# Kernel tuning notes

Hardware: AMD Instinct MI355X
Metric: run time of the kernel (lower is better)

## Reference

```python
import jax, jax.numpy as jnp
import numpy as np

B, N, DIM, MV = 8, 16384, 512, 8
SCALE = 0.1
EPS = 1e-5


def _cayley():
    # Cl(3,0) basis order: 1, e1, e2, e3, e12, e13, e23, e123 (bitmasks below)
    masks = [0b000, 0b001, 0b010, 0b100, 0b011, 0b101, 0b110, 0b111]
    idx = {m: i for i, m in enumerate(masks)}
    C = np.zeros((8, 8, 8), dtype=np.float32)
    for i, a in enumerate(masks):
        for j, b in enumerate(masks):
            s, aa = 0, a >> 1
            while aa:  # reordering sign; Euclidean signature so squares are +1
                s += bin(aa & b).count('1')
                aa >>= 1
            C[i, j, idx[a ^ b]] = -1.0 if (s % 2) else 1.0
    return jnp.asarray(C)


def setup_inputs() -> dict:
    key = jax.random.key(0)
    ks = jax.random.split(key, 8)
    lim_in = 1.0 / np.sqrt(DIM)
    lim_out = 1.0 / np.sqrt(MV)
    x = jax.random.normal(ks[0], (B, N, DIM), dtype=jnp.float32)
    Wp = jax.random.uniform(ks[1], (MV, DIM), minval=-lim_in, maxval=lim_in, dtype=jnp.float32)
    bp = jax.random.uniform(ks[2], (MV,), minval=-lim_in, maxval=lim_in, dtype=jnp.float32)
    Wm = jax.random.uniform(ks[3], (MV, DIM), minval=-lim_in, maxval=lim_in, dtype=jnp.float32)
    bm = jax.random.uniform(ks[4], (MV,), minval=-lim_in, maxval=lim_in, dtype=jnp.float32)
    Wo = jax.random.uniform(ks[5], (DIM, MV), minval=-lim_out, maxval=lim_out, dtype=jnp.float32)
    bo = jax.random.uniform(ks[6], (DIM,), minval=-lim_out, maxval=lim_out, dtype=jnp.float32)
    gamma = jnp.ones((DIM,), dtype=jnp.float32)
    beta = jnp.zeros((DIM,), dtype=jnp.float32)
    return {"x": x, "Wp": Wp, "bp": bp, "Wm": Wm, "bm": bm,
            "Wo": Wo, "bo": bo, "gamma": gamma, "beta": beta}


def reference(x, Wp, bp, Wm, bm, Wo, bo, gamma, beta):
    C = _cayley()  # [8,8,8] sparse Cayley tensor for Cl(3,0)
    particle_mv = jnp.einsum('bnd,md->bnm', x, Wp) + bp          # [B,N,8]
    mean_field = x.mean(axis=1)                                   # [B,D]
    meanfield_mv = jnp.einsum('bd,md->bm', mean_field, Wm) + bm   # [B,8]
    # geometric product: mean-field mv is shared across N
    product = jnp.einsum('bni,ijk,bj->bnk', particle_mv, C, meanfield_mv)  # [B,N,8]
    out = jnp.einsum('bnk,dk->bnd', product, Wo) + bo             # [B,N,D]
    y = x + SCALE * out
    mu = y.mean(axis=-1, keepdims=True)
    var = y.var(axis=-1, keepdims=True)  # biased, matches torch LayerNorm
    return gamma * (y - mu) / jnp.sqrt(var + EPS) + beta
```

## Files before the change

kernel.cpp:

```cpp
#include <hip/hip_runtime.h>

#define BB 8
#define NN 16384
#define DIMD 512
#define MVV 8
#define SCALE_C 0.1f
#define EPS_C 1e-5f

typedef unsigned int u32;

__device__ __forceinline__ void load8f(const float* __restrict__ p, float* f) {
    float4 a = *(const float4*)p;
    float4 b = *(const float4*)(p + 4);
    f[0] = a.x; f[1] = a.y; f[2] = a.z; f[3] = a.w;
    f[4] = b.x; f[5] = b.y; f[6] = b.z; f[7] = b.w;
}

__global__ __launch_bounds__(256) void kzero(float* __restrict__ p, int n) {
    int i = blockIdx.x * 256 + threadIdx.x;
    if (i < n) p[i] = 0.0f;
}

__global__ __launch_bounds__(256) void kmean(const float* __restrict__ x, float* __restrict__ wsum) {
    const int b = blockIdx.y;
    const int chunk = blockIdx.x;
    const int t = threadIdx.x;
    const int c = t & 63;
    const int rt = t >> 6;
    const int rowsPerBlock = NN / 128;
    const long base = ((long)b * NN + (long)chunk * rowsPerBlock) * DIMD;

    float acc[8];
#pragma unroll
    for (int j = 0; j < 8; j++) acc[j] = 0.0f;

    for (int r = rt; r < rowsPerBlock; r += 4) {
        const float* p = x + base + (long)r * DIMD + c * 8;
        float f[8];
        load8f(p, f);
#pragma unroll
        for (int j = 0; j < 8; j++) acc[j] += f[j];
    }

    __shared__ float red[256][9];
#pragma unroll
    for (int j = 0; j < 8; j++) red[t][j] = acc[j];
    __syncthreads();

    if (t < 64) {
        float s[8];
#pragma unroll
        for (int j = 0; j < 8; j++)
            s[j] = red[t][j] + red[t + 64][j] + red[t + 128][j] + red[t + 192][j];
        float* dst = wsum + b * DIMD + t * 8;
#pragma unroll
        for (int j = 0; j < 8; j++) atomicAdd(dst + j, s[j]);
    }
}

__global__ __launch_bounds__(64) void kfold(const float* __restrict__ wsum,
                                            const float* __restrict__ Wm,
                                            const float* __restrict__ bm,
                                            const float* __restrict__ Wo,
                                            const float* __restrict__ bo,
                                            const float* __restrict__ bp,
                                            float* __restrict__ wot,
                                            float* __restrict__ c2) {
    const int b = blockIdx.x;
    const int l = threadIdx.x;
    const float invN = 1.0f / (float)NN;

    float m[8];
#pragma unroll
    for (int j = 0; j < 8; j++) m[j] = wsum[b * DIMD + l * 8 + j] * invN;

    float mf[8];
#pragma unroll
    for (int i = 0; i < 8; i++) {
        float wmr[8];
        load8f(Wm + i * DIMD + l * 8, wmr);
        float p = 0.0f;
#pragma unroll
        for (int j = 0; j < 8; j++) p += m[j] * wmr[j];
#pragma unroll
        for (int off = 32; off >= 1; off >>= 1) p += __shfl_xor(p, off, 64);
        mf[i] = p + bm[i];
    }

    const int masks[8] = {0, 1, 2, 4, 3, 5, 6, 7};
    const int invm[8]  = {0, 1, 2, 4, 3, 5, 6, 7};
    float T[8][8];
#pragma unroll
    for (int i = 0; i < 8; i++) {
#pragma unroll
        for (int k = 0; k < 8; k++) {
            int bmask = masks[i] ^ masks[k];
            int j = invm[bmask];
            int s = 0, aa = masks[i] >> 1;
            while (aa) { s += __popc(aa & bmask); aa >>= 1; }
            T[i][k] = (s & 1) ? -mf[j] : mf[j];
        }
    }

    float cv[8];
#pragma unroll
    for (int k = 0; k < 8; k++) {
        float s = 0.0f;
#pragma unroll
        for (int i = 0; i < 8; i++) s += bp[i] * T[i][k];
        cv[k] = s;
    }

#pragma unroll
    for (int j = 0; j < 8; j++) {
        int d = l * 8 + j;
        float wor[8];
        load8f(Wo + d * 8, wor);
        float cc = bo[d];
#pragma unroll
        for (int k = 0; k < 8; k++) cc += cv[k] * wor[k];
        c2[b * DIMD + d] = cc;
#pragma unroll
        for (int i = 0; i < 8; i++) {
            float s = 0.0f;
#pragma unroll
            for (int k = 0; k < 8; k++) s += T[i][k] * wor[k];
            wot[((long)b * DIMD + d) * 8 + i] = s;
        }
    }
}

__global__ __launch_bounds__(256, 2) void kmain(const float* __restrict__ x,
                                                const float* __restrict__ Wp,
                                                const float* __restrict__ gamma,
                                                const float* __restrict__ beta,
                                                const float* __restrict__ wot,
                                                const float* __restrict__ c2,
                                                float* __restrict__ out) {
    const int b = blockIdx.y;
    const int chunk = blockIdx.x;
    const int w = threadIdx.x >> 6;
    const int l = threadIdx.x & 63;
    const int d0 = l * 8;

    float wp[8][8];
#pragma unroll
    for (int i = 0; i < 8; i++) load8f(Wp + i * DIMD + d0, wp[i]);

    float wo[8][8];
    const float* wotp = wot + ((long)b * DIMD + d0) * 8;
#pragma unroll
    for (int j = 0; j < 8; j++)
#pragma unroll
        for (int i = 0; i < 8; i++) wo[j][i] = wotp[j * 8 + i];

    float cc[8];
#pragma unroll
    for (int j = 0; j < 8; j++) cc[j] = c2[b * DIMD + d0 + j];

    float g[8], be[8];
    load8f(gamma + d0, g);
    load8f(beta + d0, be);

    const int rowsPerBlock = NN / 128;
    const long rowbase = (long)b * NN + (long)chunk * rowsPerBlock;

    for (int r = w; r < rowsPerBlock; r += 4) {
        const float* px = x + (rowbase + r) * DIMD + d0;
        float xv[8];
        load8f(px, xv);

        float pm[8];
#pragma unroll
        for (int i = 0; i < 8; i++) {
            float p = xv[0] * wp[i][0];
#pragma unroll
            for (int j = 1; j < 8; j++) p += xv[j] * wp[i][j];
            pm[i] = p;
        }
#pragma unroll
        for (int off = 32; off >= 1; off >>= 1) {
#pragma unroll
            for (int i = 0; i < 8; i++) pm[i] += __shfl_xor(pm[i], off, 64);
        }

        float yv[8], s1 = 0.0f, s2 = 0.0f;
#pragma unroll
        for (int j = 0; j < 8; j++) {
            float o = cc[j];
#pragma unroll
            for (int i = 0; i < 8; i++) o += pm[i] * wo[j][i];
            float y = xv[j] + SCALE_C * o;
            yv[j] = y;
            s1 += y;
            s2 += y * y;
        }
#pragma unroll
        for (int off = 32; off >= 1; off >>= 1) {
            s1 += __shfl_xor(s1, off, 64);
            s2 += __shfl_xor(s2, off, 64);
        }
        float mu = s1 * (1.0f / DIMD);
        float var = s2 * (1.0f / DIMD) - mu * mu;
        float rs = rsqrtf(var + EPS_C);

        float ov[8];
#pragma unroll
        for (int j = 0; j < 8; j++) {
            ov[j] = g[j] * (yv[j] - mu) * rs + be[j];
        }
        float* po = out + (rowbase + r) * DIMD + d0;
        *(float4*)po = make_float4(ov[0], ov[1], ov[2], ov[3]);
        *(float4*)(po + 4) = make_float4(ov[4], ov[5], ov[6], ov[7]);
    }
}

extern "C" void kernel_launch(void* const* d_in, const int* in_sizes, int n_in,
                              void* d_out, int out_size, void* d_ws, size_t ws_size,
                              hipStream_t stream) {
    const float* x     = (const float*)d_in[0];
    const float* Wp    = (const float*)d_in[1];
    const float* bp    = (const float*)d_in[2];
    const float* Wm    = (const float*)d_in[3];
    const float* bm    = (const float*)d_in[4];
    const float* Wo    = (const float*)d_in[5];
    const float* bo    = (const float*)d_in[6];
    const float* gamma = (const float*)d_in[7];
    const float* beta  = (const float*)d_in[8];

    float* ws   = (float*)d_ws;
    float* wsum = ws;
    float* wot  = ws + 4096;
    float* c2   = ws + 4096 + 32768;

    kzero<<<16, 256, 0, stream>>>(wsum, BB * DIMD);
    kmean<<<dim3(128, 8), 256, 0, stream>>>(x, wsum);
    kfold<<<8, 64, 0, stream>>>(wsum, Wm, bm, Wo, bo, bp, wot, c2);
    kmain<<<dim3(128, 8), 256, 0, stream>>>(x, Wp, gamma, beta, wot, c2, (float*)d_out);
}
```

Measured before the change: 581.0 us.

## Use transpose-reduce butterflies, prefetch next row, nontemporal stores in main kernel

The 8 per-row projection reductions are replaced by a recursive-halving butterfly, where each shuffle stage exchanges half the values, cutting cross-lane shuffles from 48 to about 15 plus 8 broadcasts. The LayerNorm s1/s2 reductions are packed into one shuffle chain. The next row of x is software-prefetched into registers, and outputs use nontemporal stores. The mean kernel loads two rows per iteration. Together these aim to lower shuffle/ALU overhead and hide memory latency, at the cost of extra registers, which risks occupancy with launch bounds of 2 blocks per CU.

Measured after the change: 550.1 us. 1.06x faster.

```diff
diff --git a/kernel.cpp b/kernel.cpp
--- a/kernel.cpp
+++ b/kernel.cpp
@@ -8,6 +8,7 @@
 #define EPS_C 1e-5f
 
 typedef unsigned int u32;
+typedef float f32x4 __attribute__((ext_vector_type(4)));
 
 __device__ __forceinline__ void load8f(const float* __restrict__ p, float* f) {
     float4 a = *(const float4*)p;
@@ -34,12 +35,14 @@
 #pragma unroll
     for (int j = 0; j < 8; j++) acc[j] = 0.0f;
 
-    for (int r = rt; r < rowsPerBlock; r += 4) {
-        const float* p = x + base + (long)r * DIMD + c * 8;
-        float f[8];
-        load8f(p, f);
-#pragma unroll
-        for (int j = 0; j < 8; j++) acc[j] += f[j];
+    for (int r = rt; r < rowsPerBlock; r += 8) {
+        const float* p0 = x + base + (long)r * DIMD + c * 8;
+        const float* p1 = p0 + 4L * DIMD;
+        float f0[8], f1[8];
+        load8f(p0, f0);
+        load8f(p1, f1);
+#pragma unroll
+        for (int j = 0; j < 8; j++) acc[j] += f0[j] + f1[j];
     }
 
     __shared__ float red[256][9];
@@ -142,6 +145,9 @@
     const int w = threadIdx.x >> 6;
     const int l = threadIdx.x & 63;
     const int d0 = l * 8;
+    const bool b5 = (l & 32) != 0;
+    const bool b4 = (l & 16) != 0;
+    const bool b3 = (l & 8) != 0;
 
     float wp[8][8];
 #pragma unroll
@@ -165,10 +171,15 @@
     const int rowsPerBlock = NN / 128;
     const long rowbase = (long)b * NN + (long)chunk * rowsPerBlock;
 
+    float xv[8];
+    load8f(x + (rowbase + w) * DIMD + d0, xv);
+
     for (int r = w; r < rowsPerBlock; r += 4) {
-        const float* px = x + (rowbase + r) * DIMD + d0;
-        float xv[8];
-        load8f(px, xv);
+        float xn[8];
+        const int rn = r + 4;
+        if (rn < rowsPerBlock) {
+            load8f(x + (rowbase + rn) * DIMD + d0, xn);
+        }
 
         float pm[8];
 #pragma unroll
@@ -178,40 +189,72 @@
             for (int j = 1; j < 8; j++) p += xv[j] * wp[i][j];
             pm[i] = p;
         }
-#pragma unroll
-        for (int off = 32; off >= 1; off >>= 1) {
-#pragma unroll
-            for (int i = 0; i < 8; i++) pm[i] += __shfl_xor(pm[i], off, 64);
-        }
+
+        float k1[4];
+#pragma unroll
+        for (int j = 0; j < 4; j++) {
+            float send = b5 ? pm[j] : pm[j + 4];
+            float recv = __shfl_xor(send, 32, 64);
+            k1[j] = (b5 ? pm[j + 4] : pm[j]) + recv;
+        }
+        float k2[2];
+#pragma unroll
+        for (int j = 0; j < 2; j++) {
+            float send = b4 ? k1[j] : k1[j + 2];
+            float recv = __shfl_xor(send, 16, 64);
+            k2[j] = (b4 ? k1[j + 2] : k1[j]) + recv;
+        }
+        float tsend = b3 ? k2[0] : k2[1];
+        float trecv = __shfl_xor(tsend, 8, 64);
+        float t = (b3 ? k2[1] : k2[0]) + trecv;
+        t += __shfl_xor(t, 4, 64);
+        t += __shfl_xor(t, 2, 64);
+        t += __shfl_xor(t, 1, 64);
+        float pmt[8];
+#pragma unroll
+        for (int i = 0; i < 8; i++) pmt[i] = __shfl(t, i << 3, 64);
 
         float yv[8], s1 = 0.0f, s2 = 0.0f;
 #pragma unroll
         for (int j = 0; j < 8; j++) {
             float o = cc[j];
 #pragma unroll
-            for (int i = 0; i < 8; i++) o += pm[i] * wo[j][i];
+            for (int i = 0; i < 8; i++) o += pmt[i] * wo[j][i];
             float y = xv[j] + SCALE_C * o;
             yv[j] = y;
             s1 += y;
             s2 += y * y;
         }
-#pragma unroll
-        for (int off = 32; off >= 1; off >>= 1) {
-            s1 += __shfl_xor(s1, off, 64);
-            s2 += __shfl_xor(s2, off, 64);
-        }
-        float mu = s1 * (1.0f / DIMD);
-        float var = s2 * (1.0f / DIMD) - mu * mu;
+
+        float lsend = b5 ? s1 : s2;
+        float v = (b5 ? s2 : s1) + __shfl_xor(lsend, 32, 64);
+        v += __shfl_xor(v, 16, 64);
+        v += __shfl_xor(v, 8, 64);
+        v += __shfl_xor(v, 4, 64);
+        v += __shfl_xor(v, 2, 64);
+        v += __shfl_xor(v, 1, 64);
+        float vw = __shfl_xor(v, 32, 64);
+        float S1 = b5 ? vw : v;
+        float S2 = b5 ? v : vw;
+
+        float mu = S1 * (1.0f / DIMD);
+        float var = S2 * (1.0f / DIMD) - mu * mu;
         float rs = rsqrtf(var + EPS_C);
 
-        float ov[8];
-#pragma unroll
-        for (int j = 0; j < 8; j++) {
-            ov[j] = g[j] * (yv[j] - mu) * rs + be[j];
-        }
         float* po = out + (rowbase + r) * DIMD + d0;
-        *(float4*)po = make_float4(ov[0], ov[1], ov[2], ov[3]);
-        *(float4*)(po + 4) = make_float4(ov[4], ov[5], ov[6], ov[7]);
+        f32x4 o1 = { g[0] * (yv[0] - mu) * rs + be[0],
+                     g[1] * (yv[1] - mu) * rs + be[1],
+                     g[2] * (yv[2] - mu) * rs + be[2],
+                     g[3] * (yv[3] - mu) * rs + be[3] };
+        f32x4 o2 = { g[4] * (yv[4] - mu) * rs + be[4],
+                     g[5] * (yv[5] - mu) * rs + be[5],
+                     g[6] * (yv[6] - mu) * rs + be[6],
+                     g[7] * (yv[7] - mu) * rs + be[7] };
+        __builtin_nontemporal_store(o1, (f32x4*)po);
+        __builtin_nontemporal_store(o2, (f32x4*)(po + 4));
+
+#pragma unroll
+        for (int j = 0; j < 8; j++) xv[j] = xn[j];
     }
 }
 
```

## Pipeline x loads, use recursive-halving shuffles, reverse row order, nontemporal stores

Applied to the files above, without the earlier changes.

The mean kernel now issues four independent row loads per iteration to raise memory-level parallelism. The main kernel handles two rows per wave per iteration and prefetches the next pair of rows into registers. It replaces the 48 butterfly shuffles for the 8 projection sums with a recursive-halving reduce-scatter followed by broadcasts, and it packs the two LayerNorm sums into one shuffle chain. Rows are walked in reverse, so the rows most recently read by the mean kernel are likely still in cache, and output is written with nontemporal stores. Register pressure goes up and the lane-select logic adds some ALU work.

After: 526.9 us. 1.1x faster.

```diff
diff --git a/kernel.cpp b/kernel.cpp
--- a/kernel.cpp
+++ b/kernel.cpp
@@ -8,6 +8,7 @@
 #define EPS_C 1e-5f
 
 typedef unsigned int u32;
+typedef float f32x4 __attribute__((ext_vector_type(4)));
 
 __device__ __forceinline__ void load8f(const float* __restrict__ p, float* f) {
     float4 a = *(const float4*)p;
@@ -34,12 +35,15 @@
 #pragma unroll
     for (int j = 0; j < 8; j++) acc[j] = 0.0f;
 
-    for (int r = rt; r < rowsPerBlock; r += 4) {
-        const float* p = x + base + (long)r * DIMD + c * 8;
-        float f[8];
-        load8f(p, f);
-#pragma unroll
-        for (int j = 0; j < 8; j++) acc[j] += f[j];
+    for (int r = rt; r < rowsPerBlock; r += 16) {
+        const float* p0 = x + base + (long)r * DIMD + c * 8;
+        float f0[8], f1[8], f2[8], f3[8];
+        load8f(p0, f0);
+        load8f(p0 + 4L * DIMD, f1);
+        load8f(p0 + 8L * DIMD, f2);
+        load8f(p0 + 12L * DIMD, f3);
+#pragma unroll
+        for (int j = 0; j < 8; j++) acc[j] += (f0[j] + f1[j]) + (f2[j] + f3[j]);
     }
 
     __shared__ float red[256][9];
@@ -142,6 +146,9 @@
     const int w = threadIdx.x >> 6;
     const int l = threadIdx.x & 63;
     const int d0 = l * 8;
+    const bool b5 = (l & 32) != 0;
+    const bool b4 = (l & 16) != 0;
+    const bool b3 = (l & 8) != 0;
 
     float wp[8][8];
 #pragma unroll
@@ -162,56 +169,131 @@
     load8f(gamma + d0, g);
     load8f(beta + d0, be);
 
-    const int rowsPerBlock = NN / 128;
-    const long rowbase = (long)b * NN + (long)chunk * rowsPerBlock;
-
-    for (int r = w; r < rowsPerBlock; r += 4) {
-        const float* px = x + (rowbase + r) * DIMD + d0;
-        float xv[8];
-        load8f(px, xv);
-
-        float pm[8];
-#pragma unroll
-        for (int i = 0; i < 8; i++) {
-            float p = xv[0] * wp[i][0];
-#pragma unroll
-            for (int j = 1; j < 8; j++) p += xv[j] * wp[i][j];
-            pm[i] = p;
-        }
-#pragma unroll
-        for (int off = 32; off >= 1; off >>= 1) {
-#pragma unroll
-            for (int i = 0; i < 8; i++) pm[i] += __shfl_xor(pm[i], off, 64);
-        }
-
-        float yv[8], s1 = 0.0f, s2 = 0.0f;
-#pragma unroll
-        for (int j = 0; j < 8; j++) {
-            float o = cc[j];
-#pragma unroll
-            for (int i = 0; i < 8; i++) o += pm[i] * wo[j][i];
-            float y = xv[j] + SCALE_C * o;
-            yv[j] = y;
-            s1 += y;
-            s2 += y * y;
-        }
-#pragma unroll
-        for (int off = 32; off >= 1; off >>= 1) {
-            s1 += __shfl_xor(s1, off, 64);
-            s2 += __shfl_xor(s2, off, 64);
-        }
-        float mu = s1 * (1.0f / DIMD);
-        float var = s2 * (1.0f / DIMD) - mu * mu;
-        float rs = rsqrtf(var + EPS_C);
-
-        float ov[8];
-#pragma unroll
-        for (int j = 0; j < 8; j++) {
-            ov[j] = g[j] * (yv[j] - mu) * rs + be[j];
-        }
-        float* po = out + (rowbase + r) * DIMD + d0;
-        *(float4*)po = make_float4(ov[0], ov[1], ov[2], ov[3]);
-        *(float4*)(po + 4) = make_float4(ov[4], ov[5], ov[6], ov[7]);
+    const long rowbase = (long)b * NN + (long)chunk * 128;
+
+    float xv[2][8];
+    {
+        const int r = 2 * w + 8 * 15;
+        load8f(x + (rowbase + r) * DIMD + d0, xv[0]);
+        load8f(x + (rowbase + r + 1) * DIMD + d0, xv[1]);
+    }
+
+    for (int k = 15; k >= 0; k--) {
+        const int r = 2 * w + 8 * k;
+
+        float xn[2][8];
+        if (k > 0) {
+            load8f(x + (rowbase + r - 8) * DIMD + d0, xn[0]);
+            load8f(x + (rowbase + r - 7) * DIMD + d0, xn[1]);
+        }
+
+        float pm[2][8];
+#pragma unroll
+        for (int u = 0; u < 2; u++)
+#pragma unroll
+            for (int i = 0; i < 8; i++) {
+                float p = xv[u][0] * wp[i][0];
+#pragma unroll
+                for (int j = 1; j < 8; j++) p += xv[u][j] * wp[i][j];
+                pm[u][i] = p;
+            }
+
+        float k1[2][4];
+#pragma unroll
+        for (int u = 0; u < 2; u++)
+#pragma unroll
+            for (int j = 0; j < 4; j++) {
+                float send = b5 ? pm[u][j] : pm[u][j + 4];
+                float recv = __shfl_xor(send, 32, 64);
+                k1[u][j] = (b5 ? pm[u][j + 4] : pm[u][j]) + recv;
+            }
+        float k2[2][2];
+#pragma unroll
+        for (int u = 0; u < 2; u++)
+#pragma unroll
+            for (int j = 0; j < 2; j++) {
+                float send = b4 ? k1[u][j] : k1[u][j + 2];
+                float recv = __shfl_xor(send, 16, 64);
+                k2[u][j] = (b4 ? k1[u][j + 2] : k1[u][j]) + recv;
+            }
+        float t[2];
+#pragma unroll
+        for (int u = 0; u < 2; u++) {
+            float ts = b3 ? k2[u][0] : k2[u][1];
+            float tr = __shfl_xor(ts, 8, 64);
+            t[u] = (b3 ? k2[u][1] : k2[u][0]) + tr;
+        }
+#pragma unroll
+        for (int u = 0; u < 2; u++) t[u] += __shfl_xor(t[u], 4, 64);
+#pragma unroll
+        for (int u = 0; u < 2; u++) t[u] += __shfl_xor(t[u], 2, 64);
+#pragma unroll
+        for (int u = 0; u < 2; u++) t[u] += __shfl_xor(t[u], 1, 64);
+        float pmt[2][8];
+#pragma unroll
+        for (int u = 0; u < 2; u++)
+#pragma unroll
+            for (int i = 0; i < 8; i++) pmt[u][i] = __shfl(t[u], i << 3, 64);
+
+        float yv[2][8], s1[2], s2[2];
+#pragma unroll
+        for (int u = 0; u < 2; u++) {
+            s1[u] = 0.0f; s2[u] = 0.0f;
+#pragma unroll
+            for (int j = 0; j < 8; j++) {
+                float o = cc[j];
+#pragma unroll
+                for (int i = 0; i < 8; i++) o += pmt[u][i] * wo[j][i];
+                float y = xv[u][j] + SCALE_C * o;
+                yv[u][j] = y;
+                s1[u] += y;
+                s2[u] += y * y;
+            }
+        }
+
+        float v[2];
+#pragma unroll
+        for (int u = 0; u < 2; u++) {
+            float ls = b5 ? s1[u] : s2[u];
+            v[u] = (b5 ? s2[u] : s1[u]) + __shfl_xor(ls, 32, 64);
+        }
+#pragma unroll
+        for (int u = 0; u < 2; u++) v[u] += __shfl_xor(v[u], 16, 64);
+#pragma unroll
+        for (int u = 0; u < 2; u++) v[u] += __shfl_xor(v[u], 8, 64);
+#pragma unroll
+        for (int u = 0; u < 2; u++) v[u] += __shfl_xor(v[u], 4, 64);
+#pragma unroll
+        for (int u = 0; u < 2; u++) v[u] += __shfl_xor(v[u], 2, 64);
+#pragma unroll
+        for (int u = 0; u < 2; u++) v[u] += __shfl_xor(v[u], 1, 64);
+
+#pragma unroll
+        for (int u = 0; u < 2; u++) {
+            float vw = __shfl_xor(v[u], 32, 64);
+            float S1 = b5 ? vw : v[u];
+            float S2 = b5 ? v[u] : vw;
+            float mu = S1 * (1.0f / DIMD);
+            float var = S2 * (1.0f / DIMD) - mu * mu;
+            float rs = rsqrtf(var + EPS_C);
+
+            float* po = out + (rowbase + r + u) * DIMD + d0;
+            f32x4 o1 = { g[0] * (yv[u][0] - mu) * rs + be[0],
+                         g[1] * (yv[u][1] - mu) * rs + be[1],
+                         g[2] * (yv[u][2] - mu) * rs + be[2],
+                         g[3] * (yv[u][3] - mu) * rs + be[3] };
+            f32x4 o2 = { g[4] * (yv[u][4] - mu) * rs + be[4],
+                         g[5] * (yv[u][5] - mu) * rs + be[5],
+                         g[6] * (yv[u][6] - mu) * rs + be[6],
+                         g[7] * (yv[u][7] - mu) * rs + be[7] };
+            __builtin_nontemporal_store(o1, (f32x4*)po);
+            __builtin_nontemporal_store(o2, (f32x4*)(po + 4));
+        }
+
+#pragma unroll
+        for (int u = 0; u < 2; u++)
+#pragma unroll
+            for (int j = 0; j < 8; j++) xv[u][j] = xn[u][j];
     }
 }
 
```
